# Optimization experiments

Hardware: AMD Instinct MI355X
Metric: run time of the kernel (lower is better)

Reference implementation:

```python
import jax, jax.numpy as jnp
import numpy as np

B, N_PTS, M_ROIS = 2, 8192, 2048
C_IN, O, H, NS = 128, 256, 4, 32
RADIUS = 1.6
BN_EPS = 1e-5
SCALE = 10.0  # point cloud extent


def setup_inputs() -> dict:
    key = jax.random.key(0)
    ks = jax.random.split(key, 20)
    f32 = jnp.float32
    Cg = C_IN + 3  # grouper concats relative xyz to features

    def kaiming(k, shape, fan_in):
        return jax.random.normal(k, shape, f32) * np.sqrt(2.0 / fan_in)

    inp = {
        "xyz": jax.random.uniform(ks[0], (B, N_PTS, 3), f32) * SCALE,
        "new_xyz": jax.random.uniform(ks[1], (B, M_ROIS, 3), f32) * SCALE,
        "features": jax.random.normal(ks[2], (B, C_IN, N_PTS), f32),
        # conv1d (kernel=1, no bias) weights, torch layout (out, in)
        "pos_w": kaiming(ks[3], (O, 3), 3),
        "key_w": kaiming(ks[4], (O, Cg), Cg),
        "val_w1": kaiming(ks[5], (O, Cg), Cg),
        "bn1_g": jnp.ones((O,), f32), "bn1_b": jnp.zeros((O,), f32),
        "val_w2": kaiming(ks[6], (O, O), O),
        "bn2_g": jnp.ones((O,), f32), "bn2_b": jnp.zeros((O,), f32),
        "attn_w": kaiming(ks[7], (H, O), O),
        # sigmoid-gated coefficient linears (no bias)
        "kc_w": kaiming(ks[8], (O, O), O),
        "qc_w": kaiming(ks[9], (O, O), O),
        "qkc_w": kaiming(ks[10], (O, O), O),
        "vc_w": kaiming(ks[11], (O, O), O),
        # cls/reg weight MLPs: Linear(O,O//2)+ReLU, Linear(O//2,1)+Sigmoid
        "cls_w1": kaiming(ks[12], (O // 2, O), O), "cls_b1": jnp.zeros((O // 2,), f32),
        "cls_w2": kaiming(ks[13], (1, O // 2), O // 2), "cls_b2": jnp.zeros((1,), f32),
        "reg_w1": kaiming(ks[14], (O // 2, O), O), "reg_b1": jnp.zeros((O // 2,), f32),
        "reg_w2": kaiming(ks[15], (1, O // 2), O // 2), "reg_b2": jnp.zeros((1,), f32),
    }
    return inp


def _bn(x, g, b):
    # eval-mode BatchNorm1d with running_mean=0, running_var=1 (init state)
    return g[None, :, None] * (x * (1.0 / np.sqrt(1.0 + BN_EPS))) + b[None, :, None]


def _conv1x1(w, x):  # (O,C) x (M,C,NS) -> (M,O,NS)
    return jnp.einsum('oc,mcn->mon', w, x)


def _ball_group(pts, q):
    # ball query: first NS points within RADIUS of each query (pad with first hit)
    n_tot = pts.shape[0]
    d2 = jnp.sum((q[:, None, :] - pts[None, :, :]) ** 2, axis=-1)  # (M, Ntot)
    order = jnp.where(d2 < RADIUS ** 2, jnp.arange(n_tot, dtype=jnp.int32), n_tot)
    neg_vals, idx = jax.lax.top_k(-order, NS)  # smallest indices among in-ball pts
    valid = (-neg_vals) < n_tot
    idx = jnp.where(valid, idx, idx[:, :1])  # pad with first neighbor
    has_any = valid[:, :1]
    idx = jnp.where(has_any, idx, 0)  # empty balls -> point 0
    return idx, ~has_any[:, 0]


def reference(xyz, new_xyz, features, pos_w, key_w, val_w1, bn1_g, bn1_b,
              val_w2, bn2_g, bn2_b, attn_w, kc_w, qc_w, qkc_w, vc_w,
              cls_w1, cls_b1, cls_w2, cls_b2, reg_w1, reg_b1, reg_w2, reg_b2):
    pts = xyz.reshape(-1, 3)                                   # (Ntot, 3)
    feats = features.transpose(0, 2, 1).reshape(-1, C_IN)      # (Ntot, C)
    q = new_xyz.reshape(-1, 3)                                 # (M, 3)

    idx, empty_mask = _ball_group(pts, q)                      # (M, NS)
    gx = pts[idx] - q[:, None, :]                              # relative xyz (M,NS,3)
    gxt = gx.transpose(0, 2, 1)                                # (M,3,NS)
    gf = jnp.concatenate([gx, feats[idx]], axis=-1).transpose(0, 2, 1)  # (M,C+3,NS)

    pos = jax.nn.relu(_conv1x1(pos_w, gxt))                    # (M,O,NS)
    key = jax.nn.relu(_conv1x1(key_w, gf))                     # (M,O,NS)
    v = jax.nn.relu(_bn(_conv1x1(val_w1, gf), bn1_g, bn1_b))
    val = jax.nn.relu(_bn(_conv1x1(val_w2, v), bn2_g, bn2_b))  # (M,O,NS)
    pos_key = pos * key

    sig = jax.nn.sigmoid
    v_c = sig(pos.mean(2) @ vc_w.T)                            # (M,O)
    q_c = sig(pos.mean(2) @ qc_w.T)
    k_c = sig(key.mean(2) @ kc_w.T)
    qk_c = sig(pos_key.mean(2) @ qkc_w.T)

    val = val + pos * v_c[:, :, None]
    attn_emb = pos * q_c[:, :, None] + key * k_c[:, :, None] + pos_key * qk_c[:, :, None]
    attn = jax.nn.softmax(jnp.einsum('ho,mon->mhn', attn_w, attn_emb), axis=-1)  # (M,H,NS)

    m = val.shape[0]
    vh = val.reshape(m, H, O // H, NS)
    new_features = jnp.einsum('mhdn,mhn->mhd', vh, attn).reshape(m, O)  # (M,O)

    def gate(x, w1, b1, w2, b2):
        return sig(jax.nn.relu(x @ w1.T + b1) @ w2.T + b2)

    cls_features = new_features * gate(new_features, cls_w1, cls_b1, cls_w2, cls_b2)
    reg_features = new_features * gate(new_features, reg_w1, reg_b1, reg_w2, reg_b2)
    return new_features, cls_features, reg_features
```

## Files before the change

### kernel.cpp

```cpp
#include <hip/hip_runtime.h>

#define DI __device__ __forceinline__

typedef __attribute__((ext_vector_type(8))) short bf16x8;
typedef __attribute__((ext_vector_type(4))) short s16x4;
typedef __attribute__((ext_vector_type(4))) float f32x4;

DI short f2bs(float x){ unsigned u = __float_as_uint(x);
  return (short)((u + 0x7FFF + ((u >> 16) & 1)) >> 16); }
DI float bs2f(short s){ return __uint_as_float(((unsigned)(unsigned short)s) << 16); }
DI f32x4 MFMA(bf16x8 a, bf16x8 b, f32x4 c){
  return __builtin_amdgcn_mfma_f32_16x16x32_bf16(a, b, c, 0, 0, 0);
}

constexpr int NP   = 8192;
constexpr int NTOT = 16384;
constexpr int M    = 4096;
constexpr int C    = 128;
constexpr int O    = 256;
constexpr int NS   = 32;
constexpr int H    = 4;
constexpr int KP   = 160;
constexpr int GFS  = 168;
constexpr int VS   = 264;
constexpr float BNS = 0.99999500003749969f;

DI void copy_rows(short* __restrict__ dst, const short* __restrict__ src, int t){
  int row = t >> 3, s = (t & 7) * 8;
  const short* sp = src + row*VS + s;
  short* dp = dst + (size_t)row*O + s;
  #pragma unroll
  for(int j = 0; j < 4; j++)
    *(bf16x8*)(dp + j*64) = *(const bf16x8*)(sp + j*64);
}

__global__ __launch_bounds__(256) void k_prep(
    const float* __restrict__ feat,
    const float* __restrict__ kw, const float* __restrict__ v1w,
    const float* __restrict__ v2w,
    const float* __restrict__ vcw, const float* __restrict__ qcw,
    const float* __restrict__ kcw, const float* __restrict__ qkcw,
    const float* __restrict__ cw1, const float* __restrict__ rw1,
    const float* __restrict__ xyz, const float* __restrict__ nxyz,
    short* __restrict__ fT,
    short* __restrict__ keyP, short* __restrict__ v1P,
    short* __restrict__ v2b,
    short* __restrict__ gw,
    short* __restrict__ cw1b, short* __restrict__ rw1b,
    float* __restrict__ xyz4, float* __restrict__ nxyz4)
{
  __shared__ float tile[128][65];
  int blk = blockIdx.x;
  int t = threadIdx.x;
  if(blk < 256){
    int b  = blk >> 7;
    int n0 = (blk & 127) << 6;
    int nn = t & 63, c4 = t >> 6;
    const float* src = feat + (size_t)b * C * NP;
    for(int i = 0; i < 32; i++){
      int c = c4 * 32 + i;
      tile[c][nn] = src[(size_t)c * NP + n0 + nn];
    }
    __syncthreads();
    int c2 = t & 127, nb = t >> 7;
    for(int j = 0; j < 32; j++){
      int n = nb + j * 2;
      fT[((size_t)(b * NP + n0 + n)) * C + c2] = f2bs(tile[c2][n]);
    }
    return;
  }
  int i = (blk - 256) * 256 + t;
  if(i < O * KP){
    int o = i / KP, k = i % KP;
    float a = 0.0f, b = 0.0f;
    if(k < 128){ a = kw[o*131 + 3 + k]; b = v1w[o*131 + 3 + k]; }
    else if(k < 131){ a = kw[o*131 + (k - 128)]; b = v1w[o*131 + (k - 128)]; }
    keyP[i] = f2bs(a);
    v1P[i]  = f2bs(b);
  }
  if(i < O * O){
    v2b[i] = f2bs(v2w[i]);
    gw[0*O*O + i] = f2bs(vcw[i]);
    gw[1*O*O + i] = f2bs(qcw[i]);
    gw[2*O*O + i] = f2bs(kcw[i]);
    gw[3*O*O + i] = f2bs(qkcw[i]);
  }
  if(i < (O/2) * O){
    cw1b[i] = f2bs(cw1[i]);
    rw1b[i] = f2bs(rw1[i]);
  }
  if(i < NTOT){
    xyz4[i*4+0] = xyz[i*3+0];
    xyz4[i*4+1] = xyz[i*3+1];
    xyz4[i*4+2] = xyz[i*3+2];
    xyz4[i*4+3] = 0.0f;
  }
  if(i < M){
    nxyz4[i*4+0] = nxyz[i*3+0];
    nxyz4[i*4+1] = nxyz[i*3+1];
    nxyz4[i*4+2] = nxyz[i*3+2];
    nxyz4[i*4+3] = 0.0f;
  }
}

__global__ __launch_bounds__(256) void k_ballq(const float* __restrict__ xyz4,
                                               const float* __restrict__ nxyz4,
                                               int* __restrict__ idxo,
                                               float* __restrict__ gxo){
#pragma clang fp contract(off)
  int m = blockIdx.x;
  int t = threadIdx.x;
  int w = t >> 6, lane = t & 63;
  float qx = nxyz4[m*4+0], qy = nxyz4[m*4+1], qz = nxyz4[m*4+2];
  __shared__ int sel[NS];
  __shared__ int wcnt[2][4];
  int cnt = 0;
  int par = 0;
  for(int base = 0; base < NTOT; base += 256){
    int p = base + t;
    const float4 pt = *(const float4*)(xyz4 + (size_t)p*4);
    float dx = qx - pt.x, dy = qy - pt.y, dz = qz - pt.z;
    float d2 = dx*dx + dy*dy;
    d2 = d2 + dz*dz;
    bool pred = d2 < 2.56f;
    unsigned long long bal = __ballot(pred);
    if(lane == 0) wcnt[par][w] = __popcll(bal);
    __syncthreads();
    int c0 = wcnt[par][0], c1 = wcnt[par][1], c2 = wcnt[par][2], c3 = wcnt[par][3];
    int off = cnt + ((w > 0) ? c0 : 0) + ((w > 1) ? c1 : 0) + ((w > 2) ? c2 : 0);
    if(pred){
      int pos = off + __popcll(bal & ((1ull << lane) - 1ull));
      if(pos < NS) sel[pos] = p;
    }
    cnt += c0 + c1 + c2 + c3;
    par ^= 1;
    if(cnt >= NS) break;
  }
  __syncthreads();
  if(t < NS){
    int s = 0;
    if(cnt > 0) s = (t < cnt) ? sel[t] : sel[0];
    idxo[m*NS + t] = s;
    const float4 ps = *(const float4*)(xyz4 + (size_t)s*4);
    gxo[(m*NS+t)*3+0] = ps.x - qx;
    gxo[(m*NS+t)*3+1] = ps.y - qy;
    gxo[(m*NS+t)*3+2] = ps.z - qz;
  }
}

__global__ __launch_bounds__(256, 5) void k_conv(
    const short* __restrict__ fT,
    const short* __restrict__ keyP, const short* __restrict__ v1P,
    const short* __restrict__ v2b,
    const float* __restrict__ posw,
    const float* __restrict__ g1, const float* __restrict__ b1,
    const float* __restrict__ g2, const float* __restrict__ b2,
    const int* __restrict__ idxw, const float* __restrict__ gxw,
    short* __restrict__ keyo, short* __restrict__ valo,
    float* __restrict__ mPos, float* __restrict__ mKey, float* __restrict__ mPK,
    int q0)
{
  int lq = blockIdx.x, q = q0 + lq, t = threadIdx.x;
  int w = t >> 6, l = t & 63;
  int col = l & 15, kq = l >> 4;
  int ro = w * 64;
  __shared__ __align__(16) short gf[NS * GFS];
  __shared__ __align__(16) short vbuf[NS * VS];
  __shared__ float gxs[NS * 4];
  __shared__ int  sel[NS];
  if(t < NS){
    sel[t] = idxw[q*NS + t];
    gxs[t*4+0] = gxw[(q*NS+t)*3+0];
    gxs[t*4+1] = gxw[(q*NS+t)*3+1];
    gxs[t*4+2] = gxw[(q*NS+t)*3+2];
    gxs[t*4+3] = 0.0f;
  }
  __syncthreads();
  for(int i = 0; i < 8; i++){
    int n = w*8 + i;
    int p = sel[n];
    *(unsigned*)&gf[n*GFS + l*2] = *(const unsigned*)(fT + (size_t)p * C + l*2);
  }
  {
    int n = t & 31, kk = (t >> 5) * 4;
    for(int j = 0; j < 4; j++){
      int k = kk + j;
      float v = (k < 3) ? gxs[n*4 + k] : 0.0f;
      gf[n*GFS + 128 + k] = f2bs(v);
    }
  }
  __syncthreads();

  f32x4 acc[4][2];
  const f32x4 vzero = {0.0f, 0.0f, 0.0f, 0.0f};

  for(int mt=0;mt<4;mt++) for(int nt=0;nt<2;nt++) acc[mt][nt] = vzero;
  for(int ks = 0; ks < 5; ks++){
    bf16x8 b0 = *(const bf16x8*)&gf[col*GFS + ks*32 + kq*8];
    bf16x8 b1v = *(const bf16x8*)&gf[(16+col)*GFS + ks*32 + kq*8];
    for(int mt = 0; mt < 4; mt++){
      bf16x8 a = *(const bf16x8*)(keyP + (size_t)(ro + mt*16 + col)*KP + ks*32 + kq*8);
      acc[mt][0] = MFMA(a, b0, acc[mt][0]);
      acc[mt][1] = MFMA(a, b1v, acc[mt][1]);
    }
  }
  for(int mt=0;mt<4;mt++){
    for(int nt=0;nt<2;nt++){
      s16x4 pk;
      for(int r=0;r<4;r++)
        pk[r] = f2bs(fmaxf(acc[mt][nt][r], 0.0f));
      int n = nt*16 + col;
      *(s16x4*)&vbuf[n*VS + ro + mt*16 + kq*4] = pk;
    }
  }
  __syncthreads();
  copy_rows(keyo + (size_t)lq*NS*O, vbuf, t);
  for(int mt=0;mt<4;mt++){
    for(int r=0;r<4;r++){
      int o = ro + mt*16 + kq*4 + r;
      float w0 = posw[o*3+0], w1 = posw[o*3+1], w2 = posw[o*3+2];
      float sp = 0, sk = 0, spk = 0;
      for(int nt=0;nt<2;nt++){
        int n = nt*16 + col;
        float p = fmaxf(w0*gxs[n*4+0] + w1*gxs[n*4+1] + w2*gxs[n*4+2], 0.0f);
        float v = fmaxf(acc[mt][nt][r], 0.0f);
        sp += p; sk += v; spk += p*v;
      }
      for(int msk=1; msk<16; msk<<=1){
        sp += __shfl_xor(sp, msk); sk += __shfl_xor(sk, msk); spk += __shfl_xor(spk, msk);
      }
      if(col == 0){
        mPos[lq*O+o] = sp  * 0.03125f;
        mKey[lq*O+o] = sk  * 0.03125f;
        mPK [lq*O+o] = spk * 0.03125f;
      }
    }
  }

  for(int mt=0;mt<4;mt++) for(int nt=0;nt<2;nt++) acc[mt][nt] = vzero;
  for(int ks = 0; ks < 5; ks++){
    bf16x8 b0 = *(const bf16x8*)&gf[col*GFS + ks*32 + kq*8];
    bf16x8 b1v = *(const bf16x8*)&gf[(16+col)*GFS + ks*32 + kq*8];
    for(int mt = 0; mt < 4; mt++){
      bf16x8 a = *(const bf16x8*)(v1P + (size_t)(ro + mt*16 + col)*KP + ks*32 + kq*8);
      acc[mt][0] = MFMA(a, b0, acc[mt][0]);
      acc[mt][1] = MFMA(a, b1v, acc[mt][1]);
    }
  }
  __syncthreads();
  for(int mt=0;mt<4;mt++){
    int o0 = ro + mt*16 + kq*4;
    float gg[4], bb[4];
    for(int r=0;r<4;r++){ gg[r] = g1[o0+r]; bb[r] = b1[o0+r]; }
    for(int nt=0;nt<2;nt++){
      s16x4 pk;
      for(int r=0;r<4;r++)
        pk[r] = f2bs(fmaxf(gg[r]*(acc[mt][nt][r] * BNS) + bb[r], 0.0f));
      int n = nt*16 + col;
      *(s16x4*)&vbuf[n*VS + o0] = pk;
    }
  }
  __syncthreads();

  for(int mt=0;mt<4;mt++) for(int nt=0;nt<2;nt++) acc[mt][nt] = vzero;
  for(int ks = 0; ks < 8; ks++){
    bf16x8 b0 = *(const bf16x8*)&vbuf[col*VS + ks*32 + kq*8];
    bf16x8 b1v = *(const bf16x8*)&vbuf[(16+col)*VS + ks*32 + kq*8];
    for(int mt = 0; mt < 4; mt++){
      bf16x8 a = *(const bf16x8*)(v2b + (size_t)(ro + mt*16 + col)*O + ks*32 + kq*8);
      acc[mt][0] = MFMA(a, b0, acc[mt][0]);
      acc[mt][1] = MFMA(a, b1v, acc[mt][1]);
    }
  }
  s16x4 valS[4][2];
  for(int mt=0;mt<4;mt++){
    int o0 = ro + mt*16 + kq*4;
    float gg[4], bb[4];
    for(int r=0;r<4;r++){ gg[r] = g2[o0+r]; bb[r] = b2[o0+r]; }
    for(int nt=0;nt<2;nt++)
      for(int r=0;r<4;r++)
        valS[mt][nt][r] = f2bs(fmaxf(gg[r]*(acc[mt][nt][r] * BNS) + bb[r], 0.0f));
  }
  __syncthreads();
  for(int mt=0;mt<4;mt++) for(int nt=0;nt<2;nt++){
    int n = nt*16 + col;
    *(s16x4*)&vbuf[n*VS + ro + mt*16 + kq*4] = valS[mt][nt];
  }
  __syncthreads();
  copy_rows(valo + (size_t)lq*NS*O, vbuf, t);
}

__global__ __launch_bounds__(256) void k_gates(
    const float* __restrict__ mPos, const float* __restrict__ mKey,
    const float* __restrict__ mPK, const short* __restrict__ gw,
    float* __restrict__ gates)
{
  int t = threadIdx.x, w = t >> 6, l = t & 63, col = l & 15, kq = l >> 4;
  int lq0 = blockIdx.x * 16;
  const float* A  = (w < 2) ? mPos : ((w == 2) ? mKey : mPK);
  const short* Wg = gw + (size_t)w * O * O;
  f32x4 acc[16];
  const f32x4 vzero = {0.0f,0.0f,0.0f,0.0f};
  for(int i=0;i<16;i++) acc[i] = vzero;
  for(int ks = 0; ks < 8; ks++){
    union { bf16x8 v; short e[8]; } u;
    const float* ap = A + (size_t)(lq0 + col)*O + ks*32 + kq*8;
    for(int j = 0; j < 8; j++) u.e[j] = f2bs(ap[j]);
    for(int nt = 0; nt < 16; nt++){
      bf16x8 bv = *(const bf16x8*)(Wg + (size_t)(nt*16 + col)*O + ks*32 + kq*8);
      acc[nt] = MFMA(u.v, bv, acc[nt]);
    }
  }
  for(int nt=0;nt<16;nt++) for(int r=0;r<4;r++){
    int lqq = lq0 + kq*4 + r;
    int oo = nt*16 + col;
    gates[((size_t)lqq*4 + w)*O + oo] = 1.0f / (1.0f + expf(-acc[nt][r]));
  }
}

__global__ __launch_bounds__(256) void k_attn(
    const short* __restrict__ keyw, const short* __restrict__ valw,
    const float* __restrict__ gxw, const float* __restrict__ posw,
    const float* __restrict__ attw, const float* __restrict__ gates,
    float* __restrict__ outNF, int q0)
{
  int lq = blockIdx.x, q = q0 + lq, t = threadIdx.x;
  __shared__ float emL[O * 33];
  __shared__ float attnL[H * NS];
  __shared__ float gxs[NS * 3];
  __shared__ float partial[256];
  if(t < 96) gxs[t] = gxw[q*96 + t];
  float vc  = gates[((size_t)lq*4 + 0)*O + t];
  float qc  = gates[((size_t)lq*4 + 1)*O + t];
  float kc  = gates[((size_t)lq*4 + 2)*O + t];
  float qkc = gates[((size_t)lq*4 + 3)*O + t];
  float pw0 = posw[t*3+0], pw1 = posw[t*3+1], pw2 = posw[t*3+2];
  __syncthreads();
  float posr[NS];
  for(int n = 0; n < NS; n++)
    posr[n] = fmaxf(pw0*gxs[n*3] + pw1*gxs[n*3+1] + pw2*gxs[n*3+2], 0.0f);
  for(int n = 0; n < NS; n++){
    float k = bs2f(keyw[((size_t)lq*NS + n)*O + t]);
    emL[t*33 + n] = posr[n]*qc + k*kc + posr[n]*k*qkc;
  }
  __syncthreads();
  {
    int idx = t & 127, h = idx >> 5, n = idx & 31, half = t >> 7;
    float s = 0;
    const float* aw = attw + h*O + half*128;
    for(int o = 0; o < 128; o++) s += aw[o] * emL[(half*128 + o)*33 + n];
    partial[t] = s;
  }
  __syncthreads();
  if(t < 128){
    int h = t >> 5, n = t & 31;
    float s = partial[t] + partial[t + 128];
    float mx = s;
    for(int msk=1; msk<32; msk<<=1) mx = fmaxf(mx, __shfl_xor(mx, msk));
    float e = expf(s - mx);
    float sum = e;
    for(int msk=1; msk<32; msk<<=1) sum += __shfl_xor(sum, msk);
    attnL[h*NS + n] = e / sum;
  }
  __syncthreads();
  int h = t >> 6;
  float nf = 0;
  for(int n = 0; n < NS; n++){
    float v = bs2f(valw[((size_t)lq*NS + n)*O + t]);
    nf += (v + posr[n]*vc) * attnL[h*NS + n];
  }
  outNF[(size_t)q*O + t] = nf;
}

__global__ __launch_bounds__(256) void k_fgate(
    const float* __restrict__ nf,
    const short* __restrict__ cw1b, const float* __restrict__ cb1,
    const float* __restrict__ cw2, const float* __restrict__ cb2,
    const short* __restrict__ rw1b, const float* __restrict__ rb1,
    const float* __restrict__ rw2, const float* __restrict__ rb2,
    float* __restrict__ outC, float* __restrict__ outR)
{
  int t = threadIdx.x, w = t >> 6, l = t & 63, col = l & 15, kq = l >> 4;
  int q0 = blockIdx.x * 64;
  __shared__ float sC[64], sR[64];
  f32x4 acc[16];
  const f32x4 vzero = {0.0f,0.0f,0.0f,0.0f};
  for(int i=0;i<16;i++) acc[i] = vzero;
  int arow = q0 + w*16 + col;
  for(int ks = 0; ks < 8; ks++){
    union { bf16x8 v; short e[8]; } u;
    const float* ap = nf + (size_t)arow*O + ks*32 + kq*8;
    for(int j = 0; j < 8; j++) u.e[j] = f2bs(ap[j]);
    for(int nt = 0; nt < 16; nt++){
      const short* W1 = (nt < 8) ? cw1b : rw1b;
      int j = (nt & 7)*16 + col;
      bf16x8 bv = *(const bf16x8*)(W1 + (size_t)j*O + ks*32 + kq*8);
      acc[nt] = MFMA(u.v, bv, acc[nt]);
    }
  }
  for(int r = 0; r < 4; r++){
    float pc = 0, pr = 0;
    for(int nt = 0; nt < 8; nt++){
      int j = nt*16 + col;
      pc += fmaxf(acc[nt][r] + cb1[j], 0.0f) * cw2[j];
    }
    for(int nt = 8; nt < 16; nt++){
      int j = (nt - 8)*16 + col;
      pr += fmaxf(acc[nt][r] + rb1[j], 0.0f) * rw2[j];
    }
    for(int msk=1; msk<16; msk<<=1){ pc += __shfl_xor(pc, msk); pr += __shfl_xor(pr, msk); }
    if(col == 0){
      int qq = w*16 + kq*4 + r;
      sC[qq] = 1.0f / (1.0f + expf(-(pc + cb2[0])));
      sR[qq] = 1.0f / (1.0f + expf(-(pr + rb2[0])));
    }
  }
  __syncthreads();
  for(int it = 0; it < 16; it++){
    int qq = it*4 + w;
    float sc = sC[qq], sr = sR[qq];
    const f32x4 nv = *(const f32x4*)(nf + (size_t)(q0 + qq)*O + l*4);
    f32x4 oc, orr;
    #pragma unroll
    for(int r=0;r<4;r++){ oc[r] = nv[r]*sc; orr[r] = nv[r]*sr; }
    *(f32x4*)(outC + (size_t)(q0 + qq)*O + l*4) = oc;
    *(f32x4*)(outR + (size_t)(q0 + qq)*O + l*4) = orr;
  }
}

extern "C" void kernel_launch(void* const* d_in, const int* in_sizes, int n_in,
                              void* d_out, int out_size, void* d_ws, size_t ws_size,
                              hipStream_t stream)
{
  const float* xyz  = (const float*)d_in[0];
  const float* nxyz = (const float*)d_in[1];
  const float* feat = (const float*)d_in[2];
  const float* posw = (const float*)d_in[3];
  const float* keyw = (const float*)d_in[4];
  const float* v1w  = (const float*)d_in[5];
  const float* bn1g = (const float*)d_in[6];
  const float* bn1b = (const float*)d_in[7];
  const float* v2w  = (const float*)d_in[8];
  const float* bn2g = (const float*)d_in[9];
  const float* bn2b = (const float*)d_in[10];
  const float* attw = (const float*)d_in[11];
  const float* kcw  = (const float*)d_in[12];
  const float* qcw  = (const float*)d_in[13];
  const float* qkcw = (const float*)d_in[14];
  const float* vcw  = (const float*)d_in[15];
  const float* cw1  = (const float*)d_in[16];
  const float* cb1  = (const float*)d_in[17];
  const float* cw2  = (const float*)d_in[18];
  const float* cb2  = (const float*)d_in[19];
  const float* rw1  = (const float*)d_in[20];
  const float* rb1  = (const float*)d_in[21];
  const float* rw2  = (const float*)d_in[22];
  const float* rb2  = (const float*)d_in[23];

  const size_t fixedB = 12000000;
  const size_t perQ   = 40960;
  int Q = 64;
  for(int cand : {4096, 2048, 1024, 512, 256, 128}){
    if(fixedB + (size_t)cand*perQ <= ws_size){ Q = cand; break; }
  }

  char* p = (char*)d_ws;
  auto alloc = [&](size_t bytes){ char* r = p; p += (bytes + 255) & ~size_t(255); return r; };
  short* fT    = (short*)alloc((size_t)NTOT*C*2);
  short* keyP  = (short*)alloc((size_t)O*KP*2);
  short* v1P   = (short*)alloc((size_t)O*KP*2);
  short* v2b   = (short*)alloc((size_t)O*O*2);
  short* gw    = (short*)alloc((size_t)4*O*O*2);
  short* cw1b  = (short*)alloc((size_t)(O/2)*O*2);
  short* rw1b  = (short*)alloc((size_t)(O/2)*O*2);
  int*   idxw  = (int*)  alloc((size_t)M*NS*4);
  float* gxw   = (float*)alloc((size_t)M*NS*3*4);
  float* xyz4  = (float*)alloc((size_t)NTOT*4*4);
  float* nxyz4 = (float*)alloc((size_t)M*4*4);
  short* keyo  = (short*)alloc((size_t)Q*NS*O*2);
  short* valo  = (short*)alloc((size_t)Q*NS*O*2);
  float* mPos  = (float*)alloc((size_t)Q*O*4);
  float* mKey  = (float*)alloc((size_t)Q*O*4);
  float* mPK   = (float*)alloc((size_t)Q*O*4);
  float* gates = (float*)alloc((size_t)Q*4*O*4);

  float* outNF = (float*)d_out;
  float* outC  = outNF + (size_t)M*O;
  float* outR  = outC  + (size_t)M*O;

  k_prep     <<<512, 256, 0, stream>>>(feat, keyw, v1w, v2w, vcw, qcw, kcw, qkcw,
                                       cw1, rw1, xyz, nxyz,
                                       fT, keyP, v1P, v2b, gw, cw1b, rw1b, xyz4, nxyz4);
  k_ballq    <<<M,   256, 0, stream>>>(xyz4, nxyz4, idxw, gxw);
  for(int q0 = 0; q0 < M; q0 += Q){
    k_conv  <<<Q,    256, 0, stream>>>(fT, keyP, v1P, v2b,
                                       posw, bn1g, bn1b, bn2g, bn2b,
                                       idxw, gxw, keyo, valo, mPos, mKey, mPK, q0);
    k_gates <<<Q/16, 256, 0, stream>>>(mPos, mKey, mPK, gw, gates);
    k_attn  <<<Q,    256, 0, stream>>>(keyo, valo, gxw, posw, attw, gates, outNF, q0);
  }
  k_fgate   <<<M/64, 256, 0, stream>>>(outNF, cw1b, cb1, cw2, cb2, rw1b, rb1, rw2, rb2, outC, outR);
}
```

Measured before the change: 363.9 us.

## Store key/val intermediates transposed and shrink attention LDS to bf16

k_conv now writes key and val activations in an (O, NS) transposed layout through a padded shared buffer. Each k_attn thread can then load its channel's 32 neighbours with four 16-byte loads instead of 32 strided scalar loads. The pooled means are stored as bf16 so k_gates loads MFMA operands directly without converting. k_attn keeps the attention embedding in bf16 shared memory, which halves its LDS footprint and may raise occupancy. The costs are extra rounding of the embedding and the means, and possible bank conflicts on the 34-element padded transposed writes.

```diff
diff --git a/kernel.cpp b/kernel.cpp
--- a/kernel.cpp
+++ b/kernel.cpp
@@ -23,16 +23,8 @@
 constexpr int KP   = 160;
 constexpr int GFS  = 168;
 constexpr int VS   = 264;
+constexpr int NSP  = 34;
 constexpr float BNS = 0.99999500003749969f;
-
-DI void copy_rows(short* __restrict__ dst, const short* __restrict__ src, int t){
-  int row = t >> 3, s = (t & 7) * 8;
-  const short* sp = src + row*VS + s;
-  short* dp = dst + (size_t)row*O + s;
-  #pragma unroll
-  for(int j = 0; j < 4; j++)
-    *(bf16x8*)(dp + j*64) = *(const bf16x8*)(sp + j*64);
-}
 
 __global__ __launch_bounds__(256) void k_prep(
     const float* __restrict__ feat,
@@ -156,8 +148,8 @@
     const float* __restrict__ g1, const float* __restrict__ b1,
     const float* __restrict__ g2, const float* __restrict__ b2,
     const int* __restrict__ idxw, const float* __restrict__ gxw,
-    short* __restrict__ keyo, short* __restrict__ valo,
-    float* __restrict__ mPos, float* __restrict__ mKey, float* __restrict__ mPK,
+    short* __restrict__ keyT, short* __restrict__ valT,
+    short* __restrict__ mPos, short* __restrict__ mKey, short* __restrict__ mPK,
     int q0)
 {
   int lq = blockIdx.x, q = q0 + lq, t = threadIdx.x;
@@ -165,7 +157,7 @@
   int col = l & 15, kq = l >> 4;
   int ro = w * 64;
   __shared__ __align__(16) short gf[NS * GFS];
-  __shared__ __align__(16) short vbuf[NS * VS];
+  __shared__ __align__(16) short buf[O * NSP];
   __shared__ float gxs[NS * 4];
   __shared__ int  sel[NS];
   if(t < NS){
@@ -204,17 +196,12 @@
       acc[mt][1] = MFMA(a, b1v, acc[mt][1]);
     }
   }
-  for(int mt=0;mt<4;mt++){
-    for(int nt=0;nt<2;nt++){
-      s16x4 pk;
-      for(int r=0;r<4;r++)
-        pk[r] = f2bs(fmaxf(acc[mt][nt][r], 0.0f));
+  for(int mt=0;mt<4;mt++) for(int nt=0;nt<2;nt++)
+    for(int r=0;r<4;r++){
+      int o = ro + mt*16 + kq*4 + r;
       int n = nt*16 + col;
-      *(s16x4*)&vbuf[n*VS + ro + mt*16 + kq*4] = pk;
-    }
-  }
-  __syncthreads();
-  copy_rows(keyo + (size_t)lq*NS*O, vbuf, t);
+      buf[o*NSP + n] = f2bs(fmaxf(acc[mt][nt][r], 0.0f));
+    }
   for(int mt=0;mt<4;mt++){
     for(int r=0;r<4;r++){
       int o = ro + mt*16 + kq*4 + r;
@@ -230,11 +217,22 @@
         sp += __shfl_xor(sp, msk); sk += __shfl_xor(sk, msk); spk += __shfl_xor(spk, msk);
       }
       if(col == 0){
-        mPos[lq*O+o] = sp  * 0.03125f;
-        mKey[lq*O+o] = sk  * 0.03125f;
-        mPK [lq*O+o] = spk * 0.03125f;
+        mPos[lq*O+o] = f2bs(sp  * 0.03125f);
+        mKey[lq*O+o] = f2bs(sk  * 0.03125f);
+        mPK [lq*O+o] = f2bs(spk * 0.03125f);
       }
     }
+  }
+  __syncthreads();
+  {
+    uint vv[16];
+    #pragma unroll
+    for(int j=0;j<16;j++) vv[j] = *(const uint*)&buf[t*NSP + j*2];
+    uint4* dst = (uint4*)(keyT + ((size_t)lq*O + t)*NS);
+    dst[0] = make_uint4(vv[0],vv[1],vv[2],vv[3]);
+    dst[1] = make_uint4(vv[4],vv[5],vv[6],vv[7]);
+    dst[2] = make_uint4(vv[8],vv[9],vv[10],vv[11]);
+    dst[3] = make_uint4(vv[12],vv[13],vv[14],vv[15]);
   }
 
   for(int mt=0;mt<4;mt++) for(int nt=0;nt<2;nt++) acc[mt][nt] = vzero;
@@ -257,58 +255,62 @@
       for(int r=0;r<4;r++)
         pk[r] = f2bs(fmaxf(gg[r]*(acc[mt][nt][r] * BNS) + bb[r], 0.0f));
       int n = nt*16 + col;
-      *(s16x4*)&vbuf[n*VS + o0] = pk;
+      *(s16x4*)&buf[n*VS + o0] = pk;
     }
   }
   __syncthreads();
 
   for(int mt=0;mt<4;mt++) for(int nt=0;nt<2;nt++) acc[mt][nt] = vzero;
   for(int ks = 0; ks < 8; ks++){
-    bf16x8 b0 = *(const bf16x8*)&vbuf[col*VS + ks*32 + kq*8];
-    bf16x8 b1v = *(const bf16x8*)&vbuf[(16+col)*VS + ks*32 + kq*8];
+    bf16x8 b0 = *(const bf16x8*)&buf[col*VS + ks*32 + kq*8];
+    bf16x8 b1v = *(const bf16x8*)&buf[(16+col)*VS + ks*32 + kq*8];
     for(int mt = 0; mt < 4; mt++){
       bf16x8 a = *(const bf16x8*)(v2b + (size_t)(ro + mt*16 + col)*O + ks*32 + kq*8);
       acc[mt][0] = MFMA(a, b0, acc[mt][0]);
       acc[mt][1] = MFMA(a, b1v, acc[mt][1]);
     }
   }
-  s16x4 valS[4][2];
+  __syncthreads();
   for(int mt=0;mt<4;mt++){
     int o0 = ro + mt*16 + kq*4;
     float gg[4], bb[4];
     for(int r=0;r<4;r++){ gg[r] = g2[o0+r]; bb[r] = b2[o0+r]; }
-    for(int nt=0;nt<2;nt++)
+    for(int nt=0;nt<2;nt++){
+      int n = nt*16 + col;
       for(int r=0;r<4;r++)
-        valS[mt][nt][r] = f2bs(fmaxf(gg[r]*(acc[mt][nt][r] * BNS) + bb[r], 0.0f));
-  }
-  __syncthreads();
-  for(int mt=0;mt<4;mt++) for(int nt=0;nt<2;nt++){
-    int n = nt*16 + col;
-    *(s16x4*)&vbuf[n*VS + ro + mt*16 + kq*4] = valS[mt][nt];
-  }
-  __syncthreads();
-  copy_rows(valo + (size_t)lq*NS*O, vbuf, t);
+        buf[(o0+r)*NSP + n] = f2bs(fmaxf(gg[r]*(acc[mt][nt][r] * BNS) + bb[r], 0.0f));
+    }
+  }
+  __syncthreads();
+  {
+    uint vv[16];
+    #pragma unroll
+    for(int j=0;j<16;j++) vv[j] = *(const uint*)&buf[t*NSP + j*2];
+    uint4* dst = (uint4*)(valT + ((size_t)lq*O + t)*NS);
+    dst[0] = make_uint4(vv[0],vv[1],vv[2],vv[3]);
+    dst[1] = make_uint4(vv[4],vv[5],vv[6],vv[7]);
+    dst[2] = make_uint4(vv[8],vv[9],vv[10],vv[11]);
+    dst[3] = make_uint4(vv[12],vv[13],vv[14],vv[15]);
+  }
 }
 
 __global__ __launch_bounds__(256) void k_gates(
-    const float* __restrict__ mPos, const float* __restrict__ mKey,
-    const float* __restrict__ mPK, const short* __restrict__ gw,
+    const short* __restrict__ mPos, const short* __restrict__ mKey,
+    const short* __restrict__ mPK, const short* __restrict__ gw,
     float* __restrict__ gates)
 {
   int t = threadIdx.x, w = t >> 6, l = t & 63, col = l & 15, kq = l >> 4;
   int lq0 = blockIdx.x * 16;
-  const float* A  = (w < 2) ? mPos : ((w == 2) ? mKey : mPK);
+  const short* A  = (w < 2) ? mPos : ((w == 2) ? mKey : mPK);
   const short* Wg = gw + (size_t)w * O * O;
   f32x4 acc[16];
   const f32x4 vzero = {0.0f,0.0f,0.0f,0.0f};
   for(int i=0;i<16;i++) acc[i] = vzero;
   for(int ks = 0; ks < 8; ks++){
-    union { bf16x8 v; short e[8]; } u;
-    const float* ap = A + (size_t)(lq0 + col)*O + ks*32 + kq*8;
-    for(int j = 0; j < 8; j++) u.e[j] = f2bs(ap[j]);
+    bf16x8 av = *(const bf16x8*)(A + (size_t)(lq0 + col)*O + ks*32 + kq*8);
     for(int nt = 0; nt < 16; nt++){
       bf16x8 bv = *(const bf16x8*)(Wg + (size_t)(nt*16 + col)*O + ks*32 + kq*8);
-      acc[nt] = MFMA(u.v, bv, acc[nt]);
+      acc[nt] = MFMA(av, bv, acc[nt]);
     }
   }
   for(int nt=0;nt<16;nt++) for(int r=0;r<4;r++){
@@ -319,13 +321,13 @@
 }
 
 __global__ __launch_bounds__(256) void k_attn(
-    const short* __restrict__ keyw, const short* __restrict__ valw,
+    const short* __restrict__ keyT, const short* __restrict__ valT,
     const float* __restrict__ gxw, const float* __restrict__ posw,
     const float* __restrict__ attw, const float* __restrict__ gates,
     float* __restrict__ outNF, int q0)
 {
   int lq = blockIdx.x, q = q0 + lq, t = threadIdx.x;
-  __shared__ float emL[O * 33];
+  __shared__ short embL[O * NSP];
   __shared__ float attnL[H * NS];
   __shared__ float gxs[NS * 3];
   __shared__ float partial[256];
@@ -337,19 +339,39 @@
   float pw0 = posw[t*3+0], pw1 = posw[t*3+1], pw2 = posw[t*3+2];
   __syncthreads();
   float posr[NS];
+  #pragma unroll
   for(int n = 0; n < NS; n++)
     posr[n] = fmaxf(pw0*gxs[n*3] + pw1*gxs[n*3+1] + pw2*gxs[n*3+2], 0.0f);
-  for(int n = 0; n < NS; n++){
-    float k = bs2f(keyw[((size_t)lq*NS + n)*O + t]);
-    emL[t*33 + n] = posr[n]*qc + k*kc + posr[n]*k*qkc;
+  {
+    const short* kp = keyT + ((size_t)lq*O + t)*NS;
+    #pragma unroll
+    for(int g = 0; g < 4; g++){
+      bf16x8 kg = *(const bf16x8*)(kp + g*8);
+      #pragma unroll
+      for(int jj = 0; jj < 4; jj++){
+        int n0 = g*8 + jj*2;
+        float kA = bs2f(kg[jj*2]),   kB = bs2f(kg[jj*2+1]);
+        float eA = posr[n0]*qc   + kA*kc + posr[n0]*kA*qkc;
+        float eB = posr[n0+1]*qc + kB*kc + posr[n0+1]*kB*qkc;
+        unsigned pk = (unsigned)(unsigned short)f2bs(eA)
+                    | ((unsigned)(unsigned short)f2bs(eB) << 16);
+        *(unsigned*)&embL[t*NSP + n0] = pk;
+      }
+    }
   }
   __syncthreads();
   {
     int idx = t & 127, h = idx >> 5, n = idx & 31, half = t >> 7;
-    float s = 0;
     const float* aw = attw + h*O + half*128;
-    for(int o = 0; o < 128; o++) s += aw[o] * emL[(half*128 + o)*33 + n];
-    partial[t] = s;
+    const short* eb = embL + (size_t)half*128*NSP + n;
+    float s0=0, s1=0, s2=0, s3=0;
+    for(int o = 0; o < 128; o += 4){
+      s0 += aw[o+0] * bs2f(eb[(o+0)*NSP]);
+      s1 += aw[o+1] * bs2f(eb[(o+1)*NSP]);
+      s2 += aw[o+2] * bs2f(eb[(o+2)*NSP]);
+      s3 += aw[o+3] * bs2f(eb[(o+3)*NSP]);
+    }
+    partial[t] = (s0 + s1) + (s2 + s3);
   }
   __syncthreads();
   if(t < 128){
@@ -363,13 +385,21 @@
     attnL[h*NS + n] = e / sum;
   }
   __syncthreads();
-  int h = t >> 6;
-  float nf = 0;
-  for(int n = 0; n < NS; n++){
-    float v = bs2f(valw[((size_t)lq*NS + n)*O + t]);
-    nf += (v + posr[n]*vc) * attnL[h*NS + n];
-  }
-  outNF[(size_t)q*O + t] = nf;
+  {
+    const short* vp = valT + ((size_t)lq*O + t)*NS;
+    int hh = t >> 6;
+    float nf = 0;
+    #pragma unroll
+    for(int g = 0; g < 4; g++){
+      bf16x8 vg = *(const bf16x8*)(vp + g*8);
+      #pragma unroll
+      for(int j = 0; j < 8; j++){
+        int n = g*8 + j;
+        nf += (bs2f(vg[j]) + posr[n]*vc) * attnL[hh*NS + n];
+      }
+    }
+    outNF[(size_t)q*O + t] = nf;
+  }
 }
 
 __global__ __launch_bounds__(256) void k_fgate(
@@ -477,11 +507,11 @@
   float* gxw   = (float*)alloc((size_t)M*NS*3*4);
   float* xyz4  = (float*)alloc((size_t)NTOT*4*4);
   float* nxyz4 = (float*)alloc((size_t)M*4*4);
-  short* keyo  = (short*)alloc((size_t)Q*NS*O*2);
-  short* valo  = (short*)alloc((size_t)Q*NS*O*2);
-  float* mPos  = (float*)alloc((size_t)Q*O*4);
-  float* mKey  = (float*)alloc((size_t)Q*O*4);
-  float* mPK   = (float*)alloc((size_t)Q*O*4);
+  short* keyT  = (short*)alloc((size_t)Q*O*NS*2);
+  short* valT  = (short*)alloc((size_t)Q*O*NS*2);
+  short* mPos  = (short*)alloc((size_t)Q*O*2);
+  short* mKey  = (short*)alloc((size_t)Q*O*2);
+  short* mPK   = (short*)alloc((size_t)Q*O*2);
   float* gates = (float*)alloc((size_t)Q*4*O*4);
 
   float* outNF = (float*)d_out;
@@ -495,9 +525,9 @@
   for(int q0 = 0; q0 < M; q0 += Q){
     k_conv  <<<Q,    256, 0, stream>>>(fT, keyP, v1P, v2b,
                                        posw, bn1g, bn1b, bn2g, bn2b,
-                                       idxw, gxw, keyo, valo, mPos, mKey, mPK, q0);
+                                       idxw, gxw, keyT, valT, mPos, mKey, mPK, q0);
     k_gates <<<Q/16, 256, 0, stream>>>(mPos, mKey, mPK, gw, gates);
-    k_attn  <<<Q,    256, 0, stream>>>(keyo, valo, gxw, posw, attw, gates, outNF, q0);
+    k_attn  <<<Q,    256, 0, stream>>>(keyT, valT, gxw, posw, attw, gates, outNF, q0);
   }
   k_fgate   <<<M/64, 256, 0, stream>>>(outNF, cw1b, cb1, cw2, cb2, rw1b, rb1, rw2, rb2, outC, outR);
 }
```

Result: no change. 363.8 us (-0.0%).
